# Kernel optimization log

Measured on AMD Instinct MI355X. Metric: run time of the kernel, lower is better.

The kernel has to match this reference:

```python
import jax, jax.numpy as jnp
import numpy as np

NUM_CODE = 1024
DIM_CODE = 256
EPS = 1e-6


def setup_inputs() -> dict:
    key = jax.random.key(0)
    kz, ke = jax.random.split(key)
    z = jax.random.normal(kz, (32, 256, 32, 32), dtype=jnp.float32)
    # torch init: uniform(-1/num_code, 1/num_code)
    emb = jax.random.uniform(ke, (NUM_CODE, DIM_CODE), dtype=jnp.float32,
                             minval=-1.0 / NUM_CODE, maxval=1.0 / NUM_CODE)
    return {"z": z, "emb": emb}


def _l2norm(x, axis=-1):
    # F.normalize(p=2): x / max(||x||, eps_torch); torch default eps=1e-12
    n = jnp.sqrt(jnp.sum(x * x, axis=axis, keepdims=True))
    return x / jnp.maximum(n, 1e-12)


def reference(z, emb):
    N, C, H, W = z.shape
    z_flat = jnp.transpose(z, (0, 2, 3, 1)).reshape(N * H * W, C)  # (T, C)
    zn = _l2norm(z_flat, axis=1)
    en = _l2norm(emb, axis=1)
    # squared euclidean distance between normalized vectors
    d = (jnp.sum(zn * zn, axis=1, keepdims=True)
         + jnp.sum(en * en, axis=1)
         - 2.0 * jnp.matmul(zn, en.T))            # (T, K)
    min_idx = jnp.argmin(d, axis=1)               # (T,)
    quant = jnp.take(emb, min_idx, axis=0)        # (T, C) — gather of RAW codebook
    quant = jnp.transpose(quant.reshape(N, H, W, C), (0, 3, 1, 2))  # NCHW
    index = min_idx.reshape(N, H, W)
    return quant, index
```

## Files before the change

kernel.cpp:

```cpp
#include <hip/hip_runtime.h>

#define NTOK 32768
#define CDIM 256
#define KCODE 1024
#define C4 64

typedef __bf16 bf16x8 __attribute__((ext_vector_type(8)));
typedef float  f32x4  __attribute__((ext_vector_type(4)));
typedef const __attribute__((address_space(1))) void* as1cvp;
typedef __attribute__((address_space(3))) void* as3vp;

__device__ __forceinline__ unsigned long long umin64(unsigned long long a, unsigned long long b) { return a < b ? a : b; }
__device__ __forceinline__ unsigned long long umax64(unsigned long long a, unsigned long long b) { return a > b ? a : b; }

__global__ void k_norm_emb(const float* __restrict__ emb,
                           float* __restrict__ en, float* __restrict__ en2,
                           __bf16* __restrict__ eh, __bf16* __restrict__ el) {
    int k = blockIdx.x;
    int l = threadIdx.x;
    float4 v = reinterpret_cast<const float4*>(emb)[k * C4 + l];
    float ss = v.x*v.x + v.y*v.y + v.z*v.z + v.w*v.w;
    #pragma unroll
    for (int o = 32; o >= 1; o >>= 1) ss += __shfl_xor(ss, o, 64);
    float den = fmaxf(sqrtf(ss), 1e-12f);
    float4 e;
    e.x = v.x / den; e.y = v.y / den; e.z = v.z / den; e.w = v.w / den;
    reinterpret_cast<float4*>(en)[k * C4 + l] = e;
    float s2 = e.x*e.x + e.y*e.y + e.z*e.z + e.w*e.w;
    #pragma unroll
    for (int o = 32; o >= 1; o >>= 1) s2 += __shfl_xor(s2, o, 64);
    if (l == 0) en2[k] = s2;

    __bf16* ehp = eh + (size_t)k * CDIM + 4 * l;
    __bf16* elp = el + (size_t)k * CDIM + 4 * l;
    float ev[4] = {e.x, e.y, e.z, e.w};
    #pragma unroll
    for (int q = 0; q < 4; ++q) {
        __bf16 h = (__bf16)ev[q];
        ehp[q] = h;
        elp[q] = (__bf16)(ev[q] - (float)h);
    }
}

__global__ void k_norm_z(const float* __restrict__ z,
                         float* __restrict__ znt, float* __restrict__ znt2) {
    __shared__ float zsb[CDIM * 32];
    __shared__ float ssp[256];
    __shared__ float dens[32];
    int tid = threadIdx.x;
    int t0  = blockIdx.x * 32;
    int n   = t0 >> 10;
    int thw0 = t0 & 1023;

    int l = tid & 31, grp = tid >> 5;
    const float* zb = z + (((size_t)(n * CDIM)) << 10) + thw0 + l;
    float ss = 0.f;
    int c0 = grp * 32;
    for (int cc = 0; cc < 32; ++cc) {
        int c = c0 + cc;
        float v = zb[((size_t)c) << 10];
        zsb[c * 32 + ((l + c) & 31)] = v;
        ss += v * v;
    }
    ssp[tid] = ss;
    __syncthreads();
    if (tid < 32) {
        float tot = 0.f;
        #pragma unroll
        for (int g = 0; g < 8; ++g) tot += ssp[g * 32 + tid];
        dens[tid] = fmaxf(sqrtf(tot), 1e-12f);
    }
    __syncthreads();

    int l2 = tid & 63, tg = tid >> 6;
    for (int it = 0; it < 8; ++it) {
        int tok = tg * 8 + it;
        float den = dens[tok];
        float s2 = 0.f;
        #pragma unroll
        for (int cq = 0; cq < 4; ++cq) {
            int c = cq * 64 + l2;
            float v = zsb[c * 32 + ((tok + c) & 31)] / den;
            znt[((size_t)(t0 + tok)) * CDIM + c] = v;
            s2 += v * v;
        }
        #pragma unroll
        for (int o = 32; o >= 1; o >>= 1) s2 += __shfl_xor(s2, o, 64);
        if (l2 == 0) znt2[t0 + tok] = s2;
    }
}

__global__ __launch_bounds__(256, 2) void k_mfma(
        const float* __restrict__ znt,
        const __bf16* __restrict__ eh, const __bf16* __restrict__ el,
        const float* __restrict__ en2g,
        const float* __restrict__ znt2, const float* __restrict__ en,
        const float* __restrict__ emb, float* __restrict__ out) {
    __shared__ __align__(16) char smem_u[69632];
    __shared__ unsigned long long t2l[64][2][2];
    __shared__ int idxs[64];
    __bf16* ebuf = reinterpret_cast<__bf16*>(smem_u);
    float*  en2s = reinterpret_cast<float*>(smem_u + 65536);
    float*  qt   = reinterpret_cast<float*>(smem_u);

    int tid = threadIdx.x;
    int l = tid & 63, wid = tid >> 6;
    int mw = wid >> 1, nw = wid & 1;
    int t0 = blockIdx.x * 64;
    int row = l & 15, kg = l >> 4;

    for (int i = tid; i < KCODE; i += 256) en2s[i] = en2g[i];

    bf16x8 ah[2][8], al_[2][8];
    #pragma unroll
    for (int mt = 0; mt < 2; ++mt) {
        size_t tok = (size_t)(t0 + mw * 32 + mt * 16 + row);
        const float* pz = znt + tok * CDIM + kg * 8;
        #pragma unroll
        for (int ks = 0; ks < 8; ++ks) {
            float f[8];
            *reinterpret_cast<float4*>(&f[0]) = *reinterpret_cast<const float4*>(pz + ks * 32);
            *reinterpret_cast<float4*>(&f[4]) = *reinterpret_cast<const float4*>(pz + ks * 32 + 4);
            bf16x8 h, lo;
            #pragma unroll
            for (int q = 0; q < 8; ++q) {
                __bf16 hv = (__bf16)f[q];
                h[q] = hv;
                lo[q] = (__bf16)(f[q] - (float)hv);
            }
            ah[mt][ks] = h; al_[mt][ks] = lo;
        }
    }

    unsigned long long b1[8], b2[8];
    #pragma unroll
    for (int i = 0; i < 8; ++i) { b1[i] = ~0ull; b2[i] = ~0ull; }

    auto stage = [&](int buf, int ch) {
        #pragma unroll
        for (int a = 0; a < 2; ++a) {
            const __bf16* src = a ? el : eh;
            #pragma unroll
            for (int i2 = 0; i2 < 4; ++i2) {
                int s = i2 * 256 + tid;
                int code = s >> 5, c16 = s & 31;
                int gslot = c16 ^ (code & 15);
                const __bf16* gp = src + ((size_t)(ch * 32 + code)) * CDIM + gslot * 8;
                __bf16* ld = ebuf + (size_t)(buf * 2 + a) * 8192 + (size_t)(i2 * 256 + wid * 64) * 8;
                __builtin_amdgcn_global_load_lds((as1cvp)gp, (as3vp)ld, 16, 0, 0);
            }
        }
    };

    stage(0, 0);
    __syncthreads();
    #pragma unroll 2
    for (int ch = 0; ch < 32; ++ch) {
        int cur = ch & 1;
        if (ch < 31) stage(cur ^ 1, ch + 1);

        const __bf16* bh_base = ebuf + (size_t)(cur * 2 + 0) * 8192;
        const __bf16* bl_base = ebuf + (size_t)(cur * 2 + 1) * 8192;

        f32x4 a0[2], a1[2], a2[2];
        #pragma unroll
        for (int mt = 0; mt < 2; ++mt)
            #pragma unroll
            for (int r = 0; r < 4; ++r) { a0[mt][r] = 0.f; a1[mt][r] = 0.f; a2[mt][r] = 0.f; }

        int code_l = nw * 16 + row;
        #pragma unroll
        for (int ks = 0; ks < 8; ++ks) {
            int slot = (ks * 4 + kg) ^ row;
            bf16x8 bh = *reinterpret_cast<const bf16x8*>(bh_base + code_l * 256 + slot * 8);
            bf16x8 bl = *reinterpret_cast<const bf16x8*>(bl_base + code_l * 256 + slot * 8);
            #pragma unroll
            for (int mt = 0; mt < 2; ++mt) {
                a0[mt] = __builtin_amdgcn_mfma_f32_16x16x32_bf16(ah[mt][ks],  bh, a0[mt], 0, 0, 0);
                a1[mt] = __builtin_amdgcn_mfma_f32_16x16x32_bf16(ah[mt][ks],  bl, a1[mt], 0, 0, 0);
                a2[mt] = __builtin_amdgcn_mfma_f32_16x16x32_bf16(al_[mt][ks], bh, a2[mt], 0, 0, 0);
            }
        }

        int code = ch * 32 + code_l;
        float e2v = en2s[code];
        #pragma unroll
        for (int mt = 0; mt < 2; ++mt)
            #pragma unroll
            for (int r = 0; r < 4; ++r) {
                float d = fmaf(-2.0f, (a0[mt][r] + a1[mt][r]) + a2[mt][r], e2v);
                unsigned ub = __float_as_uint(d);
                ub = (ub & 0x80000000u) ? ~ub : (ub | 0x80000000u);
                unsigned long long key = ((unsigned long long)ub << 32) | (unsigned)code;
                int idx = mt * 4 + r;
                if (key < b1[idx]) { b2[idx] = b1[idx]; b1[idx] = key; }
                else if (key < b2[idx]) { b2[idx] = key; }
            }
        __syncthreads();
    }

    #pragma unroll
    for (int i = 0; i < 8; ++i) {
        #pragma unroll
        for (int off = 1; off < 16; off <<= 1) {
            unsigned long long o1 = __shfl_xor(b1[i], off, 16);
            unsigned long long o2 = __shfl_xor(b2[i], off, 16);
            unsigned long long m1 = umin64(b1[i], o1);
            unsigned long long m2 = umin64(umax64(b1[i], o1), umin64(b2[i], o2));
            b1[i] = m1; b2[i] = m2;
        }
    }
    if ((l & 15) == 0) {
        #pragma unroll
        for (int mt = 0; mt < 2; ++mt)
            #pragma unroll
            for (int r = 0; r < 4; ++r) {
                int tl = mw * 32 + mt * 16 + kg * 4 + r;
                t2l[tl][nw][0] = b1[mt * 4 + r];
                t2l[tl][nw][1] = b2[mt * 4 + r];
            }
    }
    __syncthreads();

    {
        int tl = tid >> 2, q = tid & 3;
        int t = t0 + tl;
        unsigned long long x1 = t2l[tl][0][0], x2 = t2l[tl][0][1];
        unsigned long long y1 = t2l[tl][1][0], y2 = t2l[tl][1][1];
        unsigned c1 = (unsigned)umin64(x1, y1);
        unsigned c2 = (unsigned)umin64(umax64(x1, y1), umin64(x2, y2));
        const float4* zp  = reinterpret_cast<const float4*>(znt) + (size_t)t  * C4 + q * 16;
        const float4* eap = reinterpret_cast<const float4*>(en)  + (size_t)c1 * C4 + q * 16;
        const float4* ebp = reinterpret_cast<const float4*>(en)  + (size_t)c2 * C4 + q * 16;
        float da = 0.f, db = 0.f;
        #pragma unroll
        for (int i = 0; i < 16; ++i) {
            float4 zv = zp[i], av = eap[i], bv = ebp[i];
            da += zv.x*av.x + zv.y*av.y + zv.z*av.z + zv.w*av.w;
            db += zv.x*bv.x + zv.y*bv.y + zv.z*bv.z + zv.w*bv.w;
        }
        da += __shfl_xor(da, 1, 4); da += __shfl_xor(da, 2, 4);
        db += __shfl_xor(db, 1, 4); db += __shfl_xor(db, 2, 4);
        if (q == 0) {
            float z2 = znt2[t];
            float d1 = (z2 + en2s[c1]) - 2.0f * da;
            float d2 = (z2 + en2s[c2]) - 2.0f * db;
            int k = (d2 < d1 || (d2 == d1 && c2 < c1)) ? (int)c2 : (int)c1;
            idxs[tl] = k;
            out[(size_t)NTOK * CDIM + t] = (float)k;
        }
    }
    __syncthreads();

    {
        int tl = tid >> 2, q = tid & 3;
        int kidx = idxs[tl];
        const float4* ep = reinterpret_cast<const float4*>(emb + (size_t)kidx * CDIM + q * 64);
        #pragma unroll
        for (int i = 0; i < 16; ++i) {
            float4 v = ep[i];
            int cb = q * 64 + i * 4;
            qt[tl * 257 + cb + 0] = v.x;
            qt[tl * 257 + cb + 1] = v.y;
            qt[tl * 257 + cb + 2] = v.z;
            qt[tl * 257 + cb + 3] = v.w;
        }
    }
    __syncthreads();

    {
        int hwo = tid & 63, cg = tid >> 6;
        int n = t0 >> 10, hw = (t0 & 1023) + hwo;
        float* ob = out + (size_t)n * (CDIM * 1024) + hw;
        #pragma unroll 8
        for (int cc = 0; cc < 64; ++cc) {
            int c = cg * 64 + cc;
            ob[(size_t)c * 1024] = qt[hwo * 257 + c];
        }
    }
}

extern "C" void kernel_launch(void* const* d_in, const int* in_sizes, int n_in,
                              void* d_out, int out_size, void* d_ws, size_t ws_size,
                              hipStream_t stream) {
    const float* z   = (const float*)d_in[0];
    const float* emb = (const float*)d_in[1];
    float* out  = (float*)d_out;

    float*  en   = (float*)d_ws;
    float*  en2  = en + (size_t)KCODE * CDIM;
    float*  znt2 = en2 + KCODE;
    __bf16* eh   = (__bf16*)(znt2 + NTOK);
    __bf16* el   = eh + (size_t)KCODE * CDIM;
    float*  znt  = (float*)(el + (size_t)KCODE * CDIM);

    k_norm_emb<<<KCODE, 64, 0, stream>>>(emb, en, en2, eh, el);
    k_norm_z<<<NTOK / 32, 256, 0, stream>>>(z, znt, znt2);
    k_mfma<<<NTOK / 64, 256, 0, stream>>>(znt, eh, el, en2, znt2, en, emb, out);
}
```

Measured before the change: 100.9 us.

## Split k_mfma work over 512 threads with one 16-token M tile per wave

The distance kernel block grows from 4 to 8 waves, and each wave now owns a single 16-token M tile instead of two. This halves the per-wave A fragments, accumulators and top-2 state, so register pressure drops and more waves can sit on a CU to hide LDS and global latency. The staging, dot-product refinement and gather/transpose epilogues are re-partitioned across the 512 threads. In exchange, each B fragment read from LDS feeds half as many MFMAs, and block-wide barriers now cover more waves.

Result: slower. 106.1 us (+5.1%).

```diff
diff --git a/kernel.cpp b/kernel.cpp
--- a/kernel.cpp
+++ b/kernel.cpp
@@ -90,7 +90,7 @@
     }
 }
 
-__global__ __launch_bounds__(256, 2) void k_mfma(
+__global__ __launch_bounds__(512, 4) void k_mfma(
         const float* __restrict__ znt,
         const __bf16* __restrict__ eh, const __bf16* __restrict__ el,
         const float* __restrict__ en2g,
@@ -109,12 +109,11 @@
     int t0 = blockIdx.x * 64;
     int row = l & 15, kg = l >> 4;
 
-    for (int i = tid; i < KCODE; i += 256) en2s[i] = en2g[i];
-
-    bf16x8 ah[2][8], al_[2][8];
-    #pragma unroll
-    for (int mt = 0; mt < 2; ++mt) {
-        size_t tok = (size_t)(t0 + mw * 32 + mt * 16 + row);
+    for (int i = tid; i < KCODE; i += 512) en2s[i] = en2g[i];
+
+    bf16x8 ah[8], al_[8];
+    {
+        size_t tok = (size_t)(t0 + mw * 16 + row);
         const float* pz = znt + tok * CDIM + kg * 8;
         #pragma unroll
         for (int ks = 0; ks < 8; ++ks) {
@@ -128,25 +127,25 @@
                 h[q] = hv;
                 lo[q] = (__bf16)(f[q] - (float)hv);
             }
-            ah[mt][ks] = h; al_[mt][ks] = lo;
-        }
-    }
-
-    unsigned long long b1[8], b2[8];
-    #pragma unroll
-    for (int i = 0; i < 8; ++i) { b1[i] = ~0ull; b2[i] = ~0ull; }
+            ah[ks] = h; al_[ks] = lo;
+        }
+    }
+
+    unsigned long long b1[4], b2[4];
+    #pragma unroll
+    for (int i = 0; i < 4; ++i) { b1[i] = ~0ull; b2[i] = ~0ull; }
 
     auto stage = [&](int buf, int ch) {
         #pragma unroll
         for (int a = 0; a < 2; ++a) {
             const __bf16* src = a ? el : eh;
             #pragma unroll
-            for (int i2 = 0; i2 < 4; ++i2) {
-                int s = i2 * 256 + tid;
+            for (int i2 = 0; i2 < 2; ++i2) {
+                int s = i2 * 512 + tid;
                 int code = s >> 5, c16 = s & 31;
                 int gslot = c16 ^ (code & 15);
                 const __bf16* gp = src + ((size_t)(ch * 32 + code)) * CDIM + gslot * 8;
-                __bf16* ld = ebuf + (size_t)(buf * 2 + a) * 8192 + (size_t)(i2 * 256 + wid * 64) * 8;
+                __bf16* ld = ebuf + (size_t)(buf * 2 + a) * 8192 + (size_t)(i2 * 512 + wid * 64) * 8;
                 __builtin_amdgcn_global_load_lds((as1cvp)gp, (as3vp)ld, 16, 0, 0);
             }
         }
@@ -162,11 +161,9 @@
         const __bf16* bh_base = ebuf + (size_t)(cur * 2 + 0) * 8192;
         const __bf16* bl_base = ebuf + (size_t)(cur * 2 + 1) * 8192;
 
-        f32x4 a0[2], a1[2], a2[2];
-        #pragma unroll
-        for (int mt = 0; mt < 2; ++mt)
-            #pragma unroll
-            for (int r = 0; r < 4; ++r) { a0[mt][r] = 0.f; a1[mt][r] = 0.f; a2[mt][r] = 0.f; }
+        f32x4 a0, a1, a2;
+        #pragma unroll
+        for (int r = 0; r < 4; ++r) { a0[r] = 0.f; a1[r] = 0.f; a2[r] = 0.f; }
 
         int code_l = nw * 16 + row;
         #pragma unroll
@@ -174,33 +171,27 @@
             int slot = (ks * 4 + kg) ^ row;
             bf16x8 bh = *reinterpret_cast<const bf16x8*>(bh_base + code_l * 256 + slot * 8);
             bf16x8 bl = *reinterpret_cast<const bf16x8*>(bl_base + code_l * 256 + slot * 8);
-            #pragma unroll
-            for (int mt = 0; mt < 2; ++mt) {
-                a0[mt] = __builtin_amdgcn_mfma_f32_16x16x32_bf16(ah[mt][ks],  bh, a0[mt], 0, 0, 0);
-                a1[mt] = __builtin_amdgcn_mfma_f32_16x16x32_bf16(ah[mt][ks],  bl, a1[mt], 0, 0, 0);
-                a2[mt] = __builtin_amdgcn_mfma_f32_16x16x32_bf16(al_[mt][ks], bh, a2[mt], 0, 0, 0);
-            }
+            a0 = __builtin_amdgcn_mfma_f32_16x16x32_bf16(ah[ks],  bh, a0, 0, 0, 0);
+            a1 = __builtin_amdgcn_mfma_f32_16x16x32_bf16(ah[ks],  bl, a1, 0, 0, 0);
+            a2 = __builtin_amdgcn_mfma_f32_16x16x32_bf16(al_[ks], bh, a2, 0, 0, 0);
         }
 
         int code = ch * 32 + code_l;
         float e2v = en2s[code];
         #pragma unroll
-        for (int mt = 0; mt < 2; ++mt)
-            #pragma unroll
-            for (int r = 0; r < 4; ++r) {
-                float d = fmaf(-2.0f, (a0[mt][r] + a1[mt][r]) + a2[mt][r], e2v);
-                unsigned ub = __float_as_uint(d);
-                ub = (ub & 0x80000000u) ? ~ub : (ub | 0x80000000u);
-                unsigned long long key = ((unsigned long long)ub << 32) | (unsigned)code;
-                int idx = mt * 4 + r;
-                if (key < b1[idx]) { b2[idx] = b1[idx]; b1[idx] = key; }
-                else if (key < b2[idx]) { b2[idx] = key; }
-            }
+        for (int r = 0; r < 4; ++r) {
+            float d = fmaf(-2.0f, (a0[r] + a1[r]) + a2[r], e2v);
+            unsigned ub = __float_as_uint(d);
+            ub = (ub & 0x80000000u) ? ~ub : (ub | 0x80000000u);
+            unsigned long long key = ((unsigned long long)ub << 32) | (unsigned)code;
+            if (key < b1[r]) { b2[r] = b1[r]; b1[r] = key; }
+            else if (key < b2[r]) { b2[r] = key; }
+        }
         __syncthreads();
     }
 
     #pragma unroll
-    for (int i = 0; i < 8; ++i) {
+    for (int i = 0; i < 4; ++i) {
         #pragma unroll
         for (int off = 1; off < 16; off <<= 1) {
             unsigned long long o1 = __shfl_xor(b1[i], off, 16);
@@ -212,35 +203,33 @@
     }
     if ((l & 15) == 0) {
         #pragma unroll
-        for (int mt = 0; mt < 2; ++mt)
-            #pragma unroll
-            for (int r = 0; r < 4; ++r) {
-                int tl = mw * 32 + mt * 16 + kg * 4 + r;
-                t2l[tl][nw][0] = b1[mt * 4 + r];
-                t2l[tl][nw][1] = b2[mt * 4 + r];
-            }
-    }
-    __syncthreads();
-
-    {
-        int tl = tid >> 2, q = tid & 3;
+        for (int r = 0; r < 4; ++r) {
+            int tl = mw * 16 + kg * 4 + r;
+            t2l[tl][nw][0] = b1[r];
+            t2l[tl][nw][1] = b2[r];
+        }
+    }
+    __syncthreads();
+
+    {
+        int tl = tid >> 3, q = tid & 7;
         int t = t0 + tl;
         unsigned long long x1 = t2l[tl][0][0], x2 = t2l[tl][0][1];
         unsigned long long y1 = t2l[tl][1][0], y2 = t2l[tl][1][1];
         unsigned c1 = (unsigned)umin64(x1, y1);
         unsigned c2 = (unsigned)umin64(umax64(x1, y1), umin64(x2, y2));
-        const float4* zp  = reinterpret_cast<const float4*>(znt) + (size_t)t  * C4 + q * 16;
-        const float4* eap = reinterpret_cast<const float4*>(en)  + (size_t)c1 * C4 + q * 16;
-        const float4* ebp = reinterpret_cast<const float4*>(en)  + (size_t)c2 * C4 + q * 16;
+        const float4* zp  = reinterpret_cast<const float4*>(znt) + (size_t)t  * C4 + q * 8;
+        const float4* eap = reinterpret_cast<const float4*>(en)  + (size_t)c1 * C4 + q * 8;
+        const float4* ebp = reinterpret_cast<const float4*>(en)  + (size_t)c2 * C4 + q * 8;
         float da = 0.f, db = 0.f;
         #pragma unroll
-        for (int i = 0; i < 16; ++i) {
+        for (int i = 0; i < 8; ++i) {
             float4 zv = zp[i], av = eap[i], bv = ebp[i];
             da += zv.x*av.x + zv.y*av.y + zv.z*av.z + zv.w*av.w;
             db += zv.x*bv.x + zv.y*bv.y + zv.z*bv.z + zv.w*bv.w;
         }
-        da += __shfl_xor(da, 1, 4); da += __shfl_xor(da, 2, 4);
-        db += __shfl_xor(db, 1, 4); db += __shfl_xor(db, 2, 4);
+        da += __shfl_xor(da, 1, 8); da += __shfl_xor(da, 2, 8); da += __shfl_xor(da, 4, 8);
+        db += __shfl_xor(db, 1, 8); db += __shfl_xor(db, 2, 8); db += __shfl_xor(db, 4, 8);
         if (q == 0) {
             float z2 = znt2[t];
             float d1 = (z2 + en2s[c1]) - 2.0f * da;
@@ -253,13 +242,13 @@
     __syncthreads();
 
     {
-        int tl = tid >> 2, q = tid & 3;
+        int tl = tid & 63, q = tid >> 6;
         int kidx = idxs[tl];
-        const float4* ep = reinterpret_cast<const float4*>(emb + (size_t)kidx * CDIM + q * 64);
-        #pragma unroll
-        for (int i = 0; i < 16; ++i) {
+        const float4* ep = reinterpret_cast<const float4*>(emb + (size_t)kidx * CDIM + q * 32);
+        #pragma unroll
+        for (int i = 0; i < 8; ++i) {
             float4 v = ep[i];
-            int cb = q * 64 + i * 4;
+            int cb = q * 32 + i * 4;
             qt[tl * 257 + cb + 0] = v.x;
             qt[tl * 257 + cb + 1] = v.y;
             qt[tl * 257 + cb + 2] = v.z;
@@ -273,8 +262,8 @@
         int n = t0 >> 10, hw = (t0 & 1023) + hwo;
         float* ob = out + (size_t)n * (CDIM * 1024) + hw;
         #pragma unroll 8
-        for (int cc = 0; cc < 64; ++cc) {
-            int c = cg * 64 + cc;
+        for (int cc = 0; cc < 32; ++cc) {
+            int c = cg * 32 + cc;
             ob[(size_t)c * 1024] = qt[hwo * 257 + c];
         }
     }
@@ -296,5 +285,5 @@
 
     k_norm_emb<<<KCODE, 64, 0, stream>>>(emb, en, en2, eh, el);
     k_norm_z<<<NTOK / 32, 256, 0, stream>>>(z, znt, znt2);
-    k_mfma<<<NTOK / 64, 256, 0, stream>>>(znt, eh, el, en2, znt2, en, emb, out);
-}
+    k_mfma<<<NTOK / 64, 512, 0, stream>>>(znt, eh, el, en2, znt2, en, emb, out);
+}
```

## Load codebook B-fragments directly from global into registers, drop LDS staging

Applied to the files above, without the earlier changes.

Removes the double-buffered global_load_lds staging of the bf16 hi/lo codebook into shared memory. Each wave now reads its MFMA B operands directly from global (L2-resident) memory into registers every chunk, and the per-chunk __syncthreads is gone. Shared memory shrinks to the output transpose buffer plus norms, which can raise occupancy. The gather-phase thread mapping also changes so lanes index tokens. The cost is redundant global reads across waves and blocks, and global load latency that is no longer hidden by prefetching.

Result: slower. 170.5 us (+69.0%).

```diff
diff --git a/kernel.cpp b/kernel.cpp
--- a/kernel.cpp
+++ b/kernel.cpp
@@ -7,8 +7,6 @@
 
 typedef __bf16 bf16x8 __attribute__((ext_vector_type(8)));
 typedef float  f32x4  __attribute__((ext_vector_type(4)));
-typedef const __attribute__((address_space(1))) void* as1cvp;
-typedef __attribute__((address_space(3))) void* as3vp;
 
 __device__ __forceinline__ unsigned long long umin64(unsigned long long a, unsigned long long b) { return a < b ? a : b; }
 __device__ __forceinline__ unsigned long long umax64(unsigned long long a, unsigned long long b) { return a > b ? a : b; }
@@ -96,12 +94,10 @@
         const float* __restrict__ en2g,
         const float* __restrict__ znt2, const float* __restrict__ en,
         const float* __restrict__ emb, float* __restrict__ out) {
-    __shared__ __align__(16) char smem_u[69632];
+    __shared__ __align__(16) float qt[64 * 257];
+    __shared__ float en2s[KCODE];
     __shared__ unsigned long long t2l[64][2][2];
     __shared__ int idxs[64];
-    __bf16* ebuf = reinterpret_cast<__bf16*>(smem_u);
-    float*  en2s = reinterpret_cast<float*>(smem_u + 65536);
-    float*  qt   = reinterpret_cast<float*>(smem_u);
 
     int tid = threadIdx.x;
     int l = tid & 63, wid = tid >> 6;
@@ -131,36 +127,26 @@
             ah[mt][ks] = h; al_[mt][ks] = lo;
         }
     }
+    __syncthreads();
 
     unsigned long long b1[8], b2[8];
     #pragma unroll
     for (int i = 0; i < 8; ++i) { b1[i] = ~0ull; b2[i] = ~0ull; }
 
-    auto stage = [&](int buf, int ch) {
-        #pragma unroll
-        for (int a = 0; a < 2; ++a) {
-            const __bf16* src = a ? el : eh;
-            #pragma unroll
-            for (int i2 = 0; i2 < 4; ++i2) {
-                int s = i2 * 256 + tid;
-                int code = s >> 5, c16 = s & 31;
-                int gslot = c16 ^ (code & 15);
-                const __bf16* gp = src + ((size_t)(ch * 32 + code)) * CDIM + gslot * 8;
-                __bf16* ld = ebuf + (size_t)(buf * 2 + a) * 8192 + (size_t)(i2 * 256 + wid * 64) * 8;
-                __builtin_amdgcn_global_load_lds((as1cvp)gp, (as3vp)ld, 16, 0, 0);
-            }
-        }
-    };
-
-    stage(0, 0);
-    __syncthreads();
-    #pragma unroll 2
+    const __bf16* ehp = eh + ((size_t)(nw * 16 + row)) * CDIM + kg * 8;
+    const __bf16* elp = el + ((size_t)(nw * 16 + row)) * CDIM + kg * 8;
+
+    #pragma unroll 1
     for (int ch = 0; ch < 32; ++ch) {
-        int cur = ch & 1;
-        if (ch < 31) stage(cur ^ 1, ch + 1);
-
-        const __bf16* bh_base = ebuf + (size_t)(cur * 2 + 0) * 8192;
-        const __bf16* bl_base = ebuf + (size_t)(cur * 2 + 1) * 8192;
+        const __bf16* eph = ehp + (size_t)ch * 32 * CDIM;
+        const __bf16* epl = elp + (size_t)ch * 32 * CDIM;
+
+        bf16x8 bh[8], bl[8];
+        #pragma unroll
+        for (int ks = 0; ks < 8; ++ks) {
+            bh[ks] = *reinterpret_cast<const bf16x8*>(eph + ks * 32);
+            bl[ks] = *reinterpret_cast<const bf16x8*>(epl + ks * 32);
+        }
 
         f32x4 a0[2], a1[2], a2[2];
         #pragma unroll
@@ -168,21 +154,17 @@
             #pragma unroll
             for (int r = 0; r < 4; ++r) { a0[mt][r] = 0.f; a1[mt][r] = 0.f; a2[mt][r] = 0.f; }
 
-        int code_l = nw * 16 + row;
         #pragma unroll
         for (int ks = 0; ks < 8; ++ks) {
-            int slot = (ks * 4 + kg) ^ row;
-            bf16x8 bh = *reinterpret_cast<const bf16x8*>(bh_base + code_l * 256 + slot * 8);
-            bf16x8 bl = *reinterpret_cast<const bf16x8*>(bl_base + code_l * 256 + slot * 8);
             #pragma unroll
             for (int mt = 0; mt < 2; ++mt) {
-                a0[mt] = __builtin_amdgcn_mfma_f32_16x16x32_bf16(ah[mt][ks],  bh, a0[mt], 0, 0, 0);
-                a1[mt] = __builtin_amdgcn_mfma_f32_16x16x32_bf16(ah[mt][ks],  bl, a1[mt], 0, 0, 0);
-                a2[mt] = __builtin_amdgcn_mfma_f32_16x16x32_bf16(al_[mt][ks], bh, a2[mt], 0, 0, 0);
-            }
-        }
-
-        int code = ch * 32 + code_l;
+                a0[mt] = __builtin_amdgcn_mfma_f32_16x16x32_bf16(ah[mt][ks],  bh[ks], a0[mt], 0, 0, 0);
+                a1[mt] = __builtin_amdgcn_mfma_f32_16x16x32_bf16(ah[mt][ks],  bl[ks], a1[mt], 0, 0, 0);
+                a2[mt] = __builtin_amdgcn_mfma_f32_16x16x32_bf16(al_[mt][ks], bh[ks], a2[mt], 0, 0, 0);
+            }
+        }
+
+        int code = ch * 32 + nw * 16 + row;
         float e2v = en2s[code];
         #pragma unroll
         for (int mt = 0; mt < 2; ++mt)
@@ -196,7 +178,6 @@
                 if (key < b1[idx]) { b2[idx] = b1[idx]; b1[idx] = key; }
                 else if (key < b2[idx]) { b2[idx] = key; }
             }
-        __syncthreads();
     }
 
     #pragma unroll
@@ -253,7 +234,7 @@
     __syncthreads();
 
     {
-        int tl = tid >> 2, q = tid & 3;
+        int tl = tid & 63, q = tid >> 6;
         int kidx = idxs[tl];
         const float4* ep = reinterpret_cast<const float4*>(emb + (size_t)kidx * CDIM + q * 64);
         #pragma unroll
```

## Fuse z normalization into MFMA kernel and use float/int top-2 tracking

Applied to the files above, without the earlier changes.

Removes the separate k_norm_z launch. Each MFMA block now loads its 64 tokens of z straight from NCHW into shared memory, normalizes them, builds the bf16 hi/lo A fragments from shared memory and writes znt for the rescoring step. This drops one kernel launch and the global round trip of znt and znt2 before the main kernel. The 64-bit packed-key top-2 tracking is replaced by separate float value and int index registers, which cuts 64-bit compares and shuffles but adds explicit tie-break logic. The prologue grows and may delay the MFMA loop, and it adds shared-memory traffic.

After: 116.3 us. +15.3%, slower.

```diff
diff --git a/kernel.cpp b/kernel.cpp
--- a/kernel.cpp
+++ b/kernel.cpp
@@ -9,9 +9,6 @@
 typedef float  f32x4  __attribute__((ext_vector_type(4)));
 typedef const __attribute__((address_space(1))) void* as1cvp;
 typedef __attribute__((address_space(3))) void* as3vp;
-
-__device__ __forceinline__ unsigned long long umin64(unsigned long long a, unsigned long long b) { return a < b ? a : b; }
-__device__ __forceinline__ unsigned long long umax64(unsigned long long a, unsigned long long b) { return a > b ? a : b; }
 
 __global__ void k_norm_emb(const float* __restrict__ emb,
                            float* __restrict__ en, float* __restrict__ en2,
@@ -42,62 +39,17 @@
     }
 }
 
-__global__ void k_norm_z(const float* __restrict__ z,
-                         float* __restrict__ znt, float* __restrict__ znt2) {
-    __shared__ float zsb[CDIM * 32];
+__global__ __launch_bounds__(256, 2) void k_mfma(
+        const float* __restrict__ z,
+        const __bf16* __restrict__ eh, const __bf16* __restrict__ el,
+        const float* __restrict__ en2g, const float* __restrict__ en,
+        const float* __restrict__ emb,
+        float* __restrict__ znt, float* __restrict__ out) {
+    __shared__ __align__(16) char smem_u[69632];
     __shared__ float ssp[256];
-    __shared__ float dens[32];
-    int tid = threadIdx.x;
-    int t0  = blockIdx.x * 32;
-    int n   = t0 >> 10;
-    int thw0 = t0 & 1023;
-
-    int l = tid & 31, grp = tid >> 5;
-    const float* zb = z + (((size_t)(n * CDIM)) << 10) + thw0 + l;
-    float ss = 0.f;
-    int c0 = grp * 32;
-    for (int cc = 0; cc < 32; ++cc) {
-        int c = c0 + cc;
-        float v = zb[((size_t)c) << 10];
-        zsb[c * 32 + ((l + c) & 31)] = v;
-        ss += v * v;
-    }
-    ssp[tid] = ss;
-    __syncthreads();
-    if (tid < 32) {
-        float tot = 0.f;
-        #pragma unroll
-        for (int g = 0; g < 8; ++g) tot += ssp[g * 32 + tid];
-        dens[tid] = fmaxf(sqrtf(tot), 1e-12f);
-    }
-    __syncthreads();
-
-    int l2 = tid & 63, tg = tid >> 6;
-    for (int it = 0; it < 8; ++it) {
-        int tok = tg * 8 + it;
-        float den = dens[tok];
-        float s2 = 0.f;
-        #pragma unroll
-        for (int cq = 0; cq < 4; ++cq) {
-            int c = cq * 64 + l2;
-            float v = zsb[c * 32 + ((tok + c) & 31)] / den;
-            znt[((size_t)(t0 + tok)) * CDIM + c] = v;
-            s2 += v * v;
-        }
-        #pragma unroll
-        for (int o = 32; o >= 1; o >>= 1) s2 += __shfl_xor(s2, o, 64);
-        if (l2 == 0) znt2[t0 + tok] = s2;
-    }
-}
-
-__global__ __launch_bounds__(256, 2) void k_mfma(
-        const float* __restrict__ znt,
-        const __bf16* __restrict__ eh, const __bf16* __restrict__ el,
-        const float* __restrict__ en2g,
-        const float* __restrict__ znt2, const float* __restrict__ en,
-        const float* __restrict__ emb, float* __restrict__ out) {
-    __shared__ __align__(16) char smem_u[69632];
-    __shared__ unsigned long long t2l[64][2][2];
+    __shared__ float den_l[64];
+    __shared__ float z2l[64];
+    __shared__ uint4 t2l[64][2];
     __shared__ int idxs[64];
     __bf16* ebuf = reinterpret_cast<__bf16*>(smem_u);
     float*  en2s = reinterpret_cast<float*>(smem_u + 65536);
@@ -108,33 +60,78 @@
     int mw = wid >> 1, nw = wid & 1;
     int t0 = blockIdx.x * 64;
     int row = l & 15, kg = l >> 4;
+    int n = t0 >> 10, hw0 = t0 & 1023;
+
+    {
+        int hwo = tid & 63, cg = tid >> 6;
+        const float* zb = z + (((size_t)(n * CDIM + cg * 64)) << 10) + hw0 + hwo;
+        float ss = 0.f;
+        #pragma unroll 16
+        for (int cc = 0; cc < 64; ++cc) {
+            float v = zb[((size_t)cc) << 10];
+            qt[hwo * 257 + cg * 64 + cc] = v;
+            ss += v * v;
+        }
+        ssp[tid] = ss;
+    }
+    __syncthreads();
+    if (tid < 64) {
+        float tot = ssp[tid] + ssp[tid + 64] + ssp[tid + 128] + ssp[tid + 192];
+        den_l[tid] = fmaxf(sqrtf(tot), 1e-12f);
+    }
+    __syncthreads();
+    {
+        int hwo = tid & 63, cg = tid >> 6;
+        float den = den_l[hwo];
+        float s2 = 0.f;
+        #pragma unroll 16
+        for (int cc = 0; cc < 64; ++cc) {
+            int ix = hwo * 257 + cg * 64 + cc;
+            float zn = qt[ix] / den;
+            qt[ix] = zn;
+            s2 += zn * zn;
+        }
+        ssp[tid] = s2;
+    }
+    __syncthreads();
+    if (tid < 64) z2l[tid] = ssp[tid] + ssp[tid + 64] + ssp[tid + 128] + ssp[tid + 192];
+    {
+        int lw = tid & 63, tw = tid >> 6;
+        #pragma unroll 4
+        for (int i = 0; i < 16; ++i) {
+            int t = i * 4 + tw;
+            float4 v;
+            v.x = qt[t * 257 + lw * 4 + 0];
+            v.y = qt[t * 257 + lw * 4 + 1];
+            v.z = qt[t * 257 + lw * 4 + 2];
+            v.w = qt[t * 257 + lw * 4 + 3];
+            *reinterpret_cast<float4*>(znt + ((size_t)(t0 + t)) * CDIM + lw * 4) = v;
+        }
+    }
+    bf16x8 ah[2][8], al_[2][8];
+    #pragma unroll
+    for (int mt = 0; mt < 2; ++mt) {
+        int tok = mw * 32 + mt * 16 + row;
+        #pragma unroll
+        for (int ks = 0; ks < 8; ++ks) {
+            bf16x8 h, lo;
+            #pragma unroll
+            for (int q = 0; q < 8; ++q) {
+                float f = qt[tok * 257 + kg * 8 + ks * 32 + q];
+                __bf16 hv = (__bf16)f;
+                h[q] = hv;
+                lo[q] = (__bf16)(f - (float)hv);
+            }
+            ah[mt][ks] = h; al_[mt][ks] = lo;
+        }
+    }
+    __syncthreads();
 
     for (int i = tid; i < KCODE; i += 256) en2s[i] = en2g[i];
 
-    bf16x8 ah[2][8], al_[2][8];
-    #pragma unroll
-    for (int mt = 0; mt < 2; ++mt) {
-        size_t tok = (size_t)(t0 + mw * 32 + mt * 16 + row);
-        const float* pz = znt + tok * CDIM + kg * 8;
-        #pragma unroll
-        for (int ks = 0; ks < 8; ++ks) {
-            float f[8];
-            *reinterpret_cast<float4*>(&f[0]) = *reinterpret_cast<const float4*>(pz + ks * 32);
-            *reinterpret_cast<float4*>(&f[4]) = *reinterpret_cast<const float4*>(pz + ks * 32 + 4);
-            bf16x8 h, lo;
-            #pragma unroll
-            for (int q = 0; q < 8; ++q) {
-                __bf16 hv = (__bf16)f[q];
-                h[q] = hv;
-                lo[q] = (__bf16)(f[q] - (float)hv);
-            }
-            ah[mt][ks] = h; al_[mt][ks] = lo;
-        }
-    }
-
-    unsigned long long b1[8], b2[8];
-    #pragma unroll
-    for (int i = 0; i < 8; ++i) { b1[i] = ~0ull; b2[i] = ~0ull; }
+    float v1f[8], v2f[8]; int i1a[8], i2a[8];
+    #pragma unroll
+    for (int i = 0; i < 8; ++i) { v1f[i] = 3.4e38f; v2f[i] = 3.4e38f; i1a[i] = 0; i2a[i] = 0; }
 
     auto stage = [&](int buf, int ch) {
         #pragma unroll
@@ -189,12 +186,14 @@
             #pragma unroll
             for (int r = 0; r < 4; ++r) {
                 float d = fmaf(-2.0f, (a0[mt][r] + a1[mt][r]) + a2[mt][r], e2v);
-                unsigned ub = __float_as_uint(d);
-                ub = (ub & 0x80000000u) ? ~ub : (ub | 0x80000000u);
-                unsigned long long key = ((unsigned long long)ub << 32) | (unsigned)code;
                 int idx = mt * 4 + r;
-                if (key < b1[idx]) { b2[idx] = b1[idx]; b1[idx] = key; }
-                else if (key < b2[idx]) { b2[idx] = key; }
+                bool lt2 = d < v2f[idx];
+                bool lt1 = d < v1f[idx];
+                if (lt2) {
+                    v2f[idx] = lt1 ? v1f[idx] : d;
+                    i2a[idx] = lt1 ? i1a[idx] : code;
+                    if (lt1) { v1f[idx] = d; i1a[idx] = code; }
+                }
             }
         __syncthreads();
     }
@@ -203,11 +202,14 @@
     for (int i = 0; i < 8; ++i) {
         #pragma unroll
         for (int off = 1; off < 16; off <<= 1) {
-            unsigned long long o1 = __shfl_xor(b1[i], off, 16);
-            unsigned long long o2 = __shfl_xor(b2[i], off, 16);
-            unsigned long long m1 = umin64(b1[i], o1);
-            unsigned long long m2 = umin64(umax64(b1[i], o1), umin64(b2[i], o2));
-            b1[i] = m1; b2[i] = m2;
+            float ov1 = __shfl_xor(v1f[i], off, 16); int oi1 = __shfl_xor(i1a[i], off, 16);
+            float ov2 = __shfl_xor(v2f[i], off, 16); int oi2 = __shfl_xor(i2a[i], off, 16);
+            bool w = (ov1 < v1f[i]) || (ov1 == v1f[i] && oi1 < i1a[i]);
+            float lv = w ? v1f[i] : ov1; int li = w ? i1a[i] : oi1;
+            float s2v = w ? ov2 : v2f[i]; int s2i = w ? oi2 : i2a[i];
+            v1f[i] = w ? ov1 : v1f[i]; i1a[i] = w ? oi1 : i1a[i];
+            bool s = (lv < s2v) || (lv == s2v && li < s2i);
+            v2f[i] = s ? lv : s2v; i2a[i] = s ? li : s2i;
         }
     }
     if ((l & 15) == 0) {
@@ -216,8 +218,9 @@
             #pragma unroll
             for (int r = 0; r < 4; ++r) {
                 int tl = mw * 32 + mt * 16 + kg * 4 + r;
-                t2l[tl][nw][0] = b1[mt * 4 + r];
-                t2l[tl][nw][1] = b2[mt * 4 + r];
+                int i = mt * 4 + r;
+                t2l[tl][nw] = make_uint4(__float_as_uint(v1f[i]), (unsigned)i1a[i],
+                                         __float_as_uint(v2f[i]), (unsigned)i2a[i]);
             }
     }
     __syncthreads();
@@ -225,10 +228,18 @@
     {
         int tl = tid >> 2, q = tid & 3;
         int t = t0 + tl;
-        unsigned long long x1 = t2l[tl][0][0], x2 = t2l[tl][0][1];
-        unsigned long long y1 = t2l[tl][1][0], y2 = t2l[tl][1][1];
-        unsigned c1 = (unsigned)umin64(x1, y1);
-        unsigned c2 = (unsigned)umin64(umax64(x1, y1), umin64(x2, y2));
+        uint4 A = t2l[tl][0], B = t2l[tl][1];
+        float av1 = __uint_as_float(A.x); int ai1 = (int)A.y;
+        float av2 = __uint_as_float(A.z); int ai2 = (int)A.w;
+        float bv1 = __uint_as_float(B.x); int bi1 = (int)B.y;
+        float bv2 = __uint_as_float(B.z); int bi2 = (int)B.w;
+        bool w = (bv1 < av1) || (bv1 == av1 && bi1 < ai1);
+        int   c1 = w ? bi1 : ai1;
+        float lv = w ? av1 : bv1; int li = w ? ai1 : bi1;
+        float wv2 = w ? bv2 : av2; int wi2 = w ? bi2 : ai2;
+        bool s = (lv < wv2) || (lv == wv2 && li < wi2);
+        int   c2 = s ? li : wi2;
+
         const float4* zp  = reinterpret_cast<const float4*>(znt) + (size_t)t  * C4 + q * 16;
         const float4* eap = reinterpret_cast<const float4*>(en)  + (size_t)c1 * C4 + q * 16;
         const float4* ebp = reinterpret_cast<const float4*>(en)  + (size_t)c2 * C4 + q * 16;
@@ -242,10 +253,10 @@
         da += __shfl_xor(da, 1, 4); da += __shfl_xor(da, 2, 4);
         db += __shfl_xor(db, 1, 4); db += __shfl_xor(db, 2, 4);
         if (q == 0) {
-            float z2 = znt2[t];
+            float z2 = z2l[tl];
             float d1 = (z2 + en2s[c1]) - 2.0f * da;
             float d2 = (z2 + en2s[c2]) - 2.0f * db;
-            int k = (d2 < d1 || (d2 == d1 && c2 < c1)) ? (int)c2 : (int)c1;
+            int k = (d2 < d1 || (d2 == d1 && c2 < c1)) ? c2 : c1;
             idxs[tl] = k;
             out[(size_t)NTOK * CDIM + t] = (float)k;
         }
@@ -253,7 +264,7 @@
     __syncthreads();
 
     {
-        int tl = tid >> 2, q = tid & 3;
+        int tl = tid & 63, q = tid >> 6;
         int kidx = idxs[tl];
         const float4* ep = reinterpret_cast<const float4*>(emb + (size_t)kidx * CDIM + q * 64);
         #pragma unroll
@@ -270,8 +281,7 @@
 
     {
         int hwo = tid & 63, cg = tid >> 6;
-        int n = t0 >> 10, hw = (t0 & 1023) + hwo;
-        float* ob = out + (size_t)n * (CDIM * 1024) + hw;
+        float* ob = out + (size_t)n * (CDIM * 1024) + hw0 + hwo;
         #pragma unroll 8
         for (int cc = 0; cc < 64; ++cc) {
             int c = cg * 64 + cc;
@@ -289,12 +299,10 @@
 
     float*  en   = (float*)d_ws;
     float*  en2  = en + (size_t)KCODE * CDIM;
-    float*  znt2 = en2 + KCODE;
-    __bf16* eh   = (__bf16*)(znt2 + NTOK);
+    __bf16* eh   = (__bf16*)(en2 + KCODE);
     __bf16* el   = eh + (size_t)KCODE * CDIM;
     float*  znt  = (float*)(el + (size_t)KCODE * CDIM);
 
     k_norm_emb<<<KCODE, 64, 0, stream>>>(emb, en, en2, eh, el);
-    k_norm_z<<<NTOK / 32, 256, 0, stream>>>(z, znt, znt2);
-    k_mfma<<<NTOK / 64, 256, 0, stream>>>(znt, eh, el, en2, znt2, en, emb, out);
+    k_mfma<<<NTOK / 64, 256, 0, stream>>>(z, eh, el, en2, en, emb, znt, out);
 }
```
